# Kernel tuning notes

Hardware: AMD Instinct MI355X
Metric: run time of the kernel (lower is better)

## Reference

```python
import jax, jax.numpy as jnp
import numpy as np

B, D, H, E = 1024, 64, 128, 8192


def setup_inputs() -> dict:
    key = jax.random.key(0)
    ks = jax.random.split(key, 10)
    def w(k, shape, fan_in):
        return jax.random.normal(k, shape, jnp.float32) / np.float32(np.sqrt(fan_in))
    return {
        "mu": jax.random.normal(ks[0], (B, D), jnp.float32),
        "current_edge_index": jax.random.randint(ks[1], (2, E), 0, B),
        "W1": w(ks[2], (D, H), D),   "b1": jnp.zeros((H,), jnp.float32),
        "W2": w(ks[3], (H, H), H),   "b2": jnp.zeros((H,), jnp.float32),
        "Ws1": w(ks[4], (2 * H, H), 2 * H), "bs1": jnp.zeros((H,), jnp.float32),
        "Ws2": w(ks[5], (H, 1), H),  "bs2": jnp.zeros((1,), jnp.float32),
        "Wg1": w(ks[6], (2 * H, H), 2 * H), "bg1": jnp.zeros((H,), jnp.float32),
        "Wg2": w(ks[7], (H, D), H), "bg2": jnp.zeros((D,), jnp.float32),
    }


def _gcn(x, W, b, src, dst, n):
    loop = jnp.arange(n)
    s = jnp.concatenate([src, loop])
    d = jnp.concatenate([dst, loop])
    deg = jax.ops.segment_sum(jnp.ones_like(s, x.dtype), d, num_segments=n)
    dinv = jax.lax.rsqrt(jnp.maximum(deg, 1e-12))
    norm = dinv[s] * dinv[d]                      # [E+n]
    xw = x @ W                                    # [n,H]
    out = jax.ops.segment_sum(xw[s] * norm[:, None], d, num_segments=n)
    return out + b


def _pairwise_scores(h, Ws1, bs1, Ws2, bs2):
    # score_mlp([h_i || h_j]) for all pairs, vectorized: split first-layer weight
    A = h @ Ws1[:H]                               # [B,H] contribution of h_i
    C = h @ Ws1[H:]                               # [B,H] contribution of h_j
    pre = jax.nn.relu(A[:, None, :] + C[None, :, :] + bs1)   # [B,B,H]
    s = (pre @ Ws2)[..., 0] + bs2[0]              # [B,B]
    up = jnp.triu(s, 1)                           # only i<j computed in original
    return up + up.T                              # symmetric, zero diagonal


def _kruskal(scores_np, n):
    iu, ju = np.triu_indices(n, 1)
    w = scores_np[iu, ju]
    order = np.argsort(-w, kind="stable")         # descending, stable like list.sort
    parent = list(range(n))
    rank = [0] * n
    def find(u):
        while parent[u] != u:
            parent[u] = parent[parent[u]]
            u = parent[u]
        return u
    edges = []
    for k in order:
        i, j = int(iu[k]), int(ju[k])
        ri, rj = find(i), find(j)
        if ri == rj:
            continue
        if rank[ri] < rank[rj]:
            parent[ri] = rj
        elif rank[ri] > rank[rj]:
            parent[rj] = ri
        else:
            parent[rj] = ri
            rank[ri] += 1
        edges.append((i, j))
        if len(edges) == n - 1:
            break
    return np.asarray(edges, dtype=np.int64)      # [n-1, 2]


def reference(mu, current_edge_index, W1, b1, W2, b2, Ws1, bs1, Ws2, bs2, Wg1, bg1, Wg2, bg2):
    src, dst = current_edge_index[0], current_edge_index[1]
    h = jax.nn.relu(_gcn(mu, W1, b1, src, dst, B))
    h = jax.nn.relu(_gcn(h, W2, b2, src, dst, B))
    scores = _pairwise_scores(h, Ws1, bs1, Ws2, bs2)          # [B,B]
    mst = _kruskal(np.asarray(scores), B)                     # [B-1,2], i<j
    ei = jnp.asarray(mst[:, 0])
    ej = jnp.asarray(mst[:, 1])
    # bidirectional edge index: src=[i,j,...], dst=[j,i,...]
    new_edge_index = jnp.stack([
        jnp.stack([ei, ej], axis=1).reshape(-1),
        jnp.stack([ej, ei], axis=1).reshape(-1),
    ], axis=0)                                                # [2, 2*(B-1)]
    hp = jnp.concatenate([h[ei], h[ej]], axis=1)              # [B-1, 2H]
    gamma = jnp.tanh(jax.nn.relu(hp @ Wg1 + bg1) @ Wg2 + bg2) # [B-1, D]
    return (new_edge_index, gamma)
```

## Files before the change

### kernel.cpp

```cpp
#include <hip/hip_runtime.h>
#include <hip/hip_bf16.h>
#include <math.h>

#define BN 1024
#define DIN 64
#define HD 128
#define EN 8192
#define SLOTS_STRIDE 64

__global__ void k_init(int* cnt, int* comp, unsigned long long* best, int* mstcnt) {
    int i = blockIdx.x * blockDim.x + threadIdx.x;
    if (i < BN) { cnt[i] = 0; comp[i] = i; best[i] = 0ull; }
    if (i == 0) *mstcnt = 0;
}

__global__ void k_fill(const int* dst, int* cnt, int* slots) {
    int e = blockIdx.x * blockDim.x + threadIdx.x;
    if (e < EN) {
        int d = dst[e];
        int p = atomicAdd(&cnt[d], 1);
        if (p < SLOTS_STRIDE) slots[d * SLOTS_STRIDE + p] = e;
    }
}

__global__ __launch_bounds__(128) void k_finish(int* slots, const int* cnt, float* dinv) {
    __shared__ int buf[128][65];
    int tid = threadIdx.x;
    int t = blockIdx.x * 128 + tid;
    int n = cnt[t];
    if (n > SLOTS_STRIDE) n = SLOTS_STRIDE;
    for (int k = 0; k < n; k++) buf[tid][k] = slots[t * SLOTS_STRIDE + k];
    for (int k = 1; k < n; k++) {
        int v = buf[tid][k];
        int q = k - 1;
        while (q >= 0 && buf[tid][q] > v) { buf[tid][q + 1] = buf[tid][q]; q--; }
        buf[tid][q + 1] = v;
    }
    for (int k = 0; k < n; k++) slots[t * SLOTS_STRIDE + k] = buf[tid][k];
    dinv[t] = 1.0f / sqrtf(fmaxf((float)(n + 1), 1e-12f));
}

__global__ __launch_bounds__(128) void k_mm(const float* x, const float* W, const float* bias,
                                            float* out, int K) {
    __shared__ float xr[HD];
    int row = blockIdx.x, col = threadIdx.x;
    if (col < K) xr[col] = x[row * K + col];
    __syncthreads();
    float acc = bias ? bias[col] : 0.0f;
    for (int k = 0; k < K; k++) acc = fmaf(xr[k], W[k * HD + col], acc);
    out[row * HD + col] = acc;
}

__global__ __launch_bounds__(128) void k_gather(const float* xw, const float* bvec, const int* src,
                                                const int* slots, const int* cnt,
                                                const float* dinv, float* hout) {
    int d = blockIdx.x, t = threadIdx.x;
    float dd = dinv[d];
    float acc = 0.0f;
    int base = d * SLOTS_STRIDE, n = cnt[d];
    if (n > SLOTS_STRIDE) n = SLOTS_STRIDE;
    for (int s = 0; s < n; s++) {
        int e = slots[base + s];
        int sn = src[e];
        acc = fmaf(xw[sn * HD + t], dinv[sn] * dd, acc);
    }
    acc = fmaf(xw[d * HD + t], dd * dd, acc);
    acc += bvec[t];
    hout[d * HD + t] = fmaxf(acc, 0.0f);
}

__global__ __launch_bounds__(256) void k_scores(const float* Aa, const float* Cc,
                                                const float* Ws2, const float* bs2v, float* S) {
    int bi = blockIdx.y, bj = blockIdx.x;
    if (bi > bj) return;
    __shared__ float As[64][68];
    __shared__ float Cs[64][68];
    __shared__ float w2[HD];
    int tid = threadIdx.x;
    int R = bi * 64, Cb = bj * 64;
    if (tid < HD) w2[tid] = Ws2[tid];
    int tx = tid & 15, ty = tid >> 4;
    float acc[4][4] = {};
    for (int half = 0; half < 2; half++) {
        int k0 = half * 64;
        __syncthreads();
        for (int idx = tid; idx < 64 * 64; idx += 256) {
            int row = idx >> 6;
            int kk = idx & 63;
            As[kk][row] = Aa[(R + row) * HD + k0 + kk];
            Cs[kk][row] = Cc[(Cb + row) * HD + k0 + kk];
        }
        __syncthreads();
        for (int kk = 0; kk < 64; kk++) {
            float4 av = *(const float4*)&As[kk][ty * 4];
            float4 cv = *(const float4*)&Cs[kk][tx * 4];
            float wk = w2[k0 + kk];
            float ar[4] = {av.x, av.y, av.z, av.w};
            float cr[4] = {cv.x, cv.y, cv.z, cv.w};
#pragma unroll
            for (int r = 0; r < 4; r++)
#pragma unroll
                for (int q = 0; q < 4; q++) {
                    float tv = fmaxf(ar[r] + cr[q], 0.0f);
                    acc[r][q] = fmaf(tv, wk, acc[r][q]);
                }
        }
    }
    float b2 = bs2v[0];
#pragma unroll
    for (int r = 0; r < 4; r++)
#pragma unroll
        for (int q = 0; q < 4; q++) {
            int gr = R + ty * 4 + r, gc = Cb + tx * 4 + q;
            float v = acc[r][q] + b2;
            if (gr < gc) { S[gr * BN + gc] = v; S[gc * BN + gr] = v; }
            else if (gr == gc) S[gr * BN + gc] = 0.0f;
        }
}

__device__ __forceinline__ unsigned long long edge_key(float w, int i, int j) {
    unsigned u = __float_as_uint(w);
    u = (u & 0x80000000u) ? ~u : (u | 0x80000000u);
    int a = i < j ? i : j, b = i < j ? j : i;
    unsigned packed = (unsigned)(a * BN + b);
    return ((unsigned long long)u << 20) | (unsigned long long)(0xFFFFFu - packed);
}

__global__ __launch_bounds__(256) void k_best(const float* S, const int* comp,
                                              unsigned long long* best) {
    int i = blockIdx.x;
    int ci = comp[i];
    unsigned long long loc = 0ull;
    for (int j = threadIdx.x; j < BN; j += 256) {
        if (comp[j] != ci) {
            unsigned long long key = edge_key(S[i * BN + j], i, j);
            if (key > loc) loc = key;
        }
    }
    __shared__ unsigned long long red[256];
    red[threadIdx.x] = loc;
    __syncthreads();
    for (int s = 128; s > 0; s >>= 1) {
        if (threadIdx.x < s) {
            unsigned long long o = red[threadIdx.x + s];
            if (o > red[threadIdx.x]) red[threadIdx.x] = o;
        }
        __syncthreads();
    }
    if (threadIdx.x == 0 && red[0]) atomicMax(&best[ci], red[0]);
}

__global__ __launch_bounds__(1024) void k_merge(int* comp, unsigned long long* best,
                                                unsigned long long* mst, int* mstcnt) {
    __shared__ int pa[BN], pb[BN];
    int c = threadIdx.x;
    int myComp = comp[c];
    bool root = (myComp == c);
    unsigned long long e = best[c];
    int t = c;
    if (root && e) {
        unsigned packed = 0xFFFFFu - (unsigned)(e & 0xFFFFFu);
        int a = packed >> 10, b = packed & 1023;
        int ca = comp[a], cb = comp[b];
        t = (ca == c) ? cb : ca;
    }
    pa[c] = (root && e) ? t : c;
    __syncthreads();
    bool mutual = root && e && (pa[t] == c);
    int p0 = pa[c];
    if (mutual && c < t) p0 = c;
    __syncthreads();
    pa[c] = p0;
    __syncthreads();
    if (root && e && !(mutual && c > t)) {
        int idx = atomicAdd(mstcnt, 1);
        mst[idx] = e;
    }
    for (int it = 0; it < 10; it++) {
        pb[c] = pa[pa[c]];
        __syncthreads();
        pa[c] = pb[c];
        __syncthreads();
    }
    comp[c] = pa[myComp];
    best[c] = 0ull;
}

__global__ __launch_bounds__(1024) void k_sort(const unsigned long long* mst, float* out, int* pairs) {
    __shared__ unsigned long long s[BN];
    int tid = threadIdx.x;
    s[tid] = (tid < BN - 1) ? mst[tid] : 0ull;
    __syncthreads();
    for (int k = 2; k <= BN; k <<= 1)
        for (int j = k >> 1; j > 0; j >>= 1) {
            int l = tid ^ j;
            if (l > tid) {
                unsigned long long x = s[tid], y = s[l];
                bool up = ((tid & k) == 0);
                if ((x > y) == up) { s[tid] = y; s[l] = x; }
            }
            __syncthreads();
        }
    if (tid < BN - 1) {
        unsigned long long key = s[BN - 1 - tid];
        unsigned packed = 0xFFFFFu - (unsigned)(key & 0xFFFFFu);
        int i = packed >> 10, j2 = packed & 1023;
        out[2 * tid] = (float)i;
        out[2 * tid + 1] = (float)j2;
        out[2046 + 2 * tid] = (float)j2;
        out[2046 + 2 * tid + 1] = (float)i;
        pairs[2 * tid] = i;
        pairs[2 * tid + 1] = j2;
    }
}

__global__ __launch_bounds__(128) void k_gamma(const float* h, const int* pairs,
                                               const float* Wg1, const float* bg1,
                                               const float* Wg2, const float* bg2, float* out) {
    int eidx = blockIdx.x;
    __shared__ float hp[2 * HD];
    __shared__ float z1[HD];
    int t = threadIdx.x;
    int i = pairs[2 * eidx], j = pairs[2 * eidx + 1];
    hp[t] = h[i * HD + t];
    hp[HD + t] = h[j * HD + t];
    __syncthreads();
    float acc = bg1[t];
    for (int k = 0; k < 2 * HD; k++) acc = fmaf(hp[k], Wg1[k * HD + t], acc);
    z1[t] = fmaxf(acc, 0.0f);
    __syncthreads();
    if (t < DIN) {
        float g = bg2[t];
        for (int k = 0; k < HD; k++) g = fmaf(z1[k], Wg2[k * DIN + t], g);
        out[4092 + eidx * DIN + t] = tanhf(g);
    }
}

extern "C" void kernel_launch(void* const* d_in, const int* in_sizes, int n_in,
                              void* d_out, int out_size, void* d_ws, size_t ws_size,
                              hipStream_t stream) {
    const float* mu  = (const float*)d_in[0];
    const int*   ei  = (const int*)d_in[1];
    const float* W1  = (const float*)d_in[2];
    const float* b1  = (const float*)d_in[3];
    const float* W2  = (const float*)d_in[4];
    const float* b2  = (const float*)d_in[5];
    const float* Ws1 = (const float*)d_in[6];
    const float* bs1 = (const float*)d_in[7];
    const float* Ws2 = (const float*)d_in[8];
    const float* bs2 = (const float*)d_in[9];
    const float* Wg1 = (const float*)d_in[10];
    const float* bg1 = (const float*)d_in[11];
    const float* Wg2 = (const float*)d_in[12];
    const float* bg2 = (const float*)d_in[13];
    float* out = (float*)d_out;

    const int* src = ei;
    const int* dst = ei + EN;

    char* ws = (char*)d_ws;
    int*   slots = (int*)(ws);
    int*   cnt   = (int*)(ws + 262144);
    float* dinv  = (float*)(ws + 266240);
    float* S     = (float*)(ws);
    float* xw    = (float*)(ws + 4194304);
    float* h1    = (float*)(ws + 4718592);
    float* h2    = (float*)(ws + 5242880);
    float* Aa    = (float*)(ws + 5767168);
    float* Cc    = (float*)(ws + 6291456);
    int*   comp  = (int*)(ws + 6815744);
    unsigned long long* best = (unsigned long long*)(ws + 6819840);
    unsigned long long* mst  = (unsigned long long*)(ws + 6828032);
    int*   mstcnt = (int*)(ws + 6836224);
    int*   pairs  = (int*)(ws + 6840320);

    k_init<<<4, 256, 0, stream>>>(cnt, comp, best, mstcnt);
    k_fill<<<EN / 256, 256, 0, stream>>>(dst, cnt, slots);
    k_finish<<<BN / 128, 128, 0, stream>>>(slots, cnt, dinv);

    k_mm<<<BN, HD, 0, stream>>>(mu, W1, nullptr, xw, DIN);
    k_gather<<<BN, HD, 0, stream>>>(xw, b1, src, slots, cnt, dinv, h1);
    k_mm<<<BN, HD, 0, stream>>>(h1, W2, nullptr, xw, HD);
    k_gather<<<BN, HD, 0, stream>>>(xw, b2, src, slots, cnt, dinv, h2);

    k_mm<<<BN, HD, 0, stream>>>(h2, Ws1, nullptr, Aa, HD);
    k_mm<<<BN, HD, 0, stream>>>(h2, Ws1 + HD * HD, bs1, Cc, HD);

    k_scores<<<dim3(16, 16), 256, 0, stream>>>(Aa, Cc, Ws2, bs2, S);

    for (int r = 0; r < 10; r++) {
        k_best<<<BN, 256, 0, stream>>>(S, comp, best);
        k_merge<<<1, 1024, 0, stream>>>(comp, best, mst, mstcnt);
    }

    k_sort<<<1, 1024, 0, stream>>>(mst, out, pairs);
    k_gamma<<<BN - 1, HD, 0, stream>>>(h2, pairs, Wg1, bg1, Wg2, bg2, out);
}
```

Before: 179.7 us.

## Fuse entire pipeline into one cooperative persistent kernel with grid syncs

Replaces roughly 30 separate kernel launches with a single cooperative kernel of 256 blocks that separates phases with grid.sync(). It also merges the two Ws1 matmuls, maps only upper-triangle score tiles to blocks, exits the Boruvka rounds early once the MST is complete, and replaces the bitonic sort with a rank-by-counting scatter. The aim is to remove launch overhead and idle blocks between dependent stages. In exchange, each grid-wide barrier has its own cost, the merge step runs on one block of 256 threads instead of 1024, and the slot sort now works in global memory.

```diff
diff --git a/kernel.cpp b/kernel.cpp
--- a/kernel.cpp
+++ b/kernel.cpp
@@ -1,298 +1,345 @@
 #include <hip/hip_runtime.h>
 #include <hip/hip_bf16.h>
+#include <hip/hip_cooperative_groups.h>
 #include <math.h>
+
+namespace cg = cooperative_groups;
 
 #define BN 1024
 #define DIN 64
 #define HD 128
 #define EN 8192
-#define SLOTS_STRIDE 64
-
-__global__ void k_init(int* cnt, int* comp, unsigned long long* best, int* mstcnt) {
-    int i = blockIdx.x * blockDim.x + threadIdx.x;
-    if (i < BN) { cnt[i] = 0; comp[i] = i; best[i] = 0ull; }
-    if (i == 0) *mstcnt = 0;
-}
-
-__global__ void k_fill(const int* dst, int* cnt, int* slots) {
-    int e = blockIdx.x * blockDim.x + threadIdx.x;
-    if (e < EN) {
-        int d = dst[e];
-        int p = atomicAdd(&cnt[d], 1);
-        if (p < SLOTS_STRIDE) slots[d * SLOTS_STRIDE + p] = e;
-    }
-}
-
-__global__ __launch_bounds__(128) void k_finish(int* slots, const int* cnt, float* dinv) {
-    __shared__ int buf[128][65];
-    int tid = threadIdx.x;
-    int t = blockIdx.x * 128 + tid;
-    int n = cnt[t];
-    if (n > SLOTS_STRIDE) n = SLOTS_STRIDE;
-    for (int k = 0; k < n; k++) buf[tid][k] = slots[t * SLOTS_STRIDE + k];
-    for (int k = 1; k < n; k++) {
-        int v = buf[tid][k];
-        int q = k - 1;
-        while (q >= 0 && buf[tid][q] > v) { buf[tid][q + 1] = buf[tid][q]; q--; }
-        buf[tid][q + 1] = v;
-    }
-    for (int k = 0; k < n; k++) slots[t * SLOTS_STRIDE + k] = buf[tid][k];
-    dinv[t] = 1.0f / sqrtf(fmaxf((float)(n + 1), 1e-12f));
-}
-
-__global__ __launch_bounds__(128) void k_mm(const float* x, const float* W, const float* bias,
-                                            float* out, int K) {
-    __shared__ float xr[HD];
-    int row = blockIdx.x, col = threadIdx.x;
-    if (col < K) xr[col] = x[row * K + col];
-    __syncthreads();
-    float acc = bias ? bias[col] : 0.0f;
-    for (int k = 0; k < K; k++) acc = fmaf(xr[k], W[k * HD + col], acc);
-    out[row * HD + col] = acc;
-}
-
-__global__ __launch_bounds__(128) void k_gather(const float* xw, const float* bvec, const int* src,
-                                                const int* slots, const int* cnt,
-                                                const float* dinv, float* hout) {
-    int d = blockIdx.x, t = threadIdx.x;
-    float dd = dinv[d];
-    float acc = 0.0f;
-    int base = d * SLOTS_STRIDE, n = cnt[d];
-    if (n > SLOTS_STRIDE) n = SLOTS_STRIDE;
-    for (int s = 0; s < n; s++) {
-        int e = slots[base + s];
-        int sn = src[e];
-        acc = fmaf(xw[sn * HD + t], dinv[sn] * dd, acc);
-    }
-    acc = fmaf(xw[d * HD + t], dd * dd, acc);
-    acc += bvec[t];
-    hout[d * HD + t] = fmaxf(acc, 0.0f);
-}
-
-__global__ __launch_bounds__(256) void k_scores(const float* Aa, const float* Cc,
-                                                const float* Ws2, const float* bs2v, float* S) {
-    int bi = blockIdx.y, bj = blockIdx.x;
-    if (bi > bj) return;
-    __shared__ float As[64][68];
-    __shared__ float Cs[64][68];
-    __shared__ float w2[HD];
-    int tid = threadIdx.x;
-    int R = bi * 64, Cb = bj * 64;
-    if (tid < HD) w2[tid] = Ws2[tid];
-    int tx = tid & 15, ty = tid >> 4;
-    float acc[4][4] = {};
-    for (int half = 0; half < 2; half++) {
-        int k0 = half * 64;
-        __syncthreads();
-        for (int idx = tid; idx < 64 * 64; idx += 256) {
-            int row = idx >> 6;
-            int kk = idx & 63;
-            As[kk][row] = Aa[(R + row) * HD + k0 + kk];
-            Cs[kk][row] = Cc[(Cb + row) * HD + k0 + kk];
-        }
-        __syncthreads();
-        for (int kk = 0; kk < 64; kk++) {
-            float4 av = *(const float4*)&As[kk][ty * 4];
-            float4 cv = *(const float4*)&Cs[kk][tx * 4];
-            float wk = w2[k0 + kk];
-            float ar[4] = {av.x, av.y, av.z, av.w};
-            float cr[4] = {cv.x, cv.y, cv.z, cv.w};
-#pragma unroll
-            for (int r = 0; r < 4; r++)
-#pragma unroll
-                for (int q = 0; q < 4; q++) {
-                    float tv = fmaxf(ar[r] + cr[q], 0.0f);
-                    acc[r][q] = fmaf(tv, wk, acc[r][q]);
-                }
-        }
-    }
-    float b2 = bs2v[0];
-#pragma unroll
-    for (int r = 0; r < 4; r++)
-#pragma unroll
-        for (int q = 0; q < 4; q++) {
-            int gr = R + ty * 4 + r, gc = Cb + tx * 4 + q;
-            float v = acc[r][q] + b2;
-            if (gr < gc) { S[gr * BN + gc] = v; S[gc * BN + gr] = v; }
-            else if (gr == gc) S[gr * BN + gc] = 0.0f;
-        }
-}
-
-__device__ __forceinline__ unsigned long long edge_key(float w, int i, int j) {
+
+typedef unsigned long long u64;
+
+struct Params {
+    const float* mu; const int* ei;
+    const float* W1; const float* b1; const float* W2; const float* b2;
+    const float* Ws1; const float* bs1; const float* Ws2; const float* bs2;
+    const float* Wg1; const float* bg1; const float* Wg2; const float* bg2;
+    float* out; char* ws;
+};
+
+struct SmemT {
+    union {
+        struct { float As[64][68]; float Cs[64][68]; float w2[HD]; } sc;
+        struct { int pa[BN]; int pb[BN]; } mg;
+        struct { float xr[4][HD]; } mm;
+        struct { float hp[2 * HD]; float z1[HD]; } gm;
+    } u;
+};
+
+__device__ __forceinline__ u64 edge_key(float w, int i, int j) {
     unsigned u = __float_as_uint(w);
     u = (u & 0x80000000u) ? ~u : (u | 0x80000000u);
     int a = i < j ? i : j, b = i < j ? j : i;
     unsigned packed = (unsigned)(a * BN + b);
-    return ((unsigned long long)u << 20) | (unsigned long long)(0xFFFFFu - packed);
-}
-
-__global__ __launch_bounds__(256) void k_best(const float* S, const int* comp,
-                                              unsigned long long* best) {
-    int i = blockIdx.x;
-    int ci = comp[i];
-    unsigned long long loc = 0ull;
-    for (int j = threadIdx.x; j < BN; j += 256) {
-        if (comp[j] != ci) {
-            unsigned long long key = edge_key(S[i * BN + j], i, j);
-            if (key > loc) loc = key;
-        }
-    }
-    __shared__ unsigned long long red[256];
-    red[threadIdx.x] = loc;
+    return ((u64)u << 20) | (u64)(0xFFFFFu - packed);
+}
+
+__device__ void mm_phase(SmemT& sm, int tid, int bid, const float* x, const float* W,
+                         const float* bias, float* out, int K) {
+    int r0 = bid * 4;
+    for (int idx = tid; idx < 4 * K; idx += 256)
+        sm.u.mm.xr[idx / K][idx % K] = x[(r0 + idx / K) * K + idx % K];
     __syncthreads();
-    for (int s = 128; s > 0; s >>= 1) {
-        if (threadIdx.x < s) {
-            unsigned long long o = red[threadIdx.x + s];
-            if (o > red[threadIdx.x]) red[threadIdx.x] = o;
-        }
-        __syncthreads();
-    }
-    if (threadIdx.x == 0 && red[0]) atomicMax(&best[ci], red[0]);
-}
-
-__global__ __launch_bounds__(1024) void k_merge(int* comp, unsigned long long* best,
-                                                unsigned long long* mst, int* mstcnt) {
-    __shared__ int pa[BN], pb[BN];
-    int c = threadIdx.x;
-    int myComp = comp[c];
-    bool root = (myComp == c);
-    unsigned long long e = best[c];
-    int t = c;
-    if (root && e) {
-        unsigned packed = 0xFFFFFu - (unsigned)(e & 0xFFFFFu);
-        int a = packed >> 10, b = packed & 1023;
-        int ca = comp[a], cb = comp[b];
-        t = (ca == c) ? cb : ca;
-    }
-    pa[c] = (root && e) ? t : c;
+    int col = tid & 127;
+    int ra = tid >> 7;
+    float b = bias ? bias[col] : 0.0f;
+    float a0 = b, a1 = b;
+    for (int k = 0; k < K; k++) {
+        float w = W[k * HD + col];
+        a0 = fmaf(sm.u.mm.xr[ra][k], w, a0);
+        a1 = fmaf(sm.u.mm.xr[ra + 2][k], w, a1);
+    }
+    out[(r0 + ra) * HD + col] = a0;
+    out[(r0 + ra + 2) * HD + col] = a1;
+}
+
+__device__ void gather_phase(int tid, int bid, const float* xwv, const float* bvec,
+                             const int* src, const int* slots, const int* cnt,
+                             const float* dinv, float* hout) {
+    int t = tid & 127;
+    for (int p = 0; p < 2; p++) {
+        int d = bid * 4 + (tid >> 7) + p * 2;
+        float dd = dinv[d];
+        float acc = 0.0f;
+        int base = d * 64, n = cnt[d];
+        if (n > 64) n = 64;
+        for (int s = 0; s < n; s++) {
+            int e = slots[base + s];
+            int sn = src[e];
+            acc = fmaf(xwv[sn * HD + t], dinv[sn] * dd, acc);
+        }
+        acc = fmaf(xwv[d * HD + t], dd * dd, acc);
+        acc += bvec[t];
+        hout[d * HD + t] = fmaxf(acc, 0.0f);
+    }
+}
+
+__device__ void merge_block(SmemT& sm, int tid, int* comp, u64* best, u64* mst, int* mstcnt) {
+    int* pa = sm.u.mg.pa;
+    int* pb = sm.u.mg.pb;
+    for (int c = tid; c < BN; c += 256) {
+        int myComp = comp[c];
+        bool root = (myComp == c);
+        u64 e = best[c];
+        int t = c;
+        if (root && e) {
+            unsigned packed = 0xFFFFFu - (unsigned)(e & 0xFFFFFu);
+            int a = packed >> 10, b = packed & 1023;
+            int ca = comp[a], cb = comp[b];
+            t = (ca == c) ? cb : ca;
+        }
+        pa[c] = (root && e) ? t : c;
+    }
     __syncthreads();
-    bool mutual = root && e && (pa[t] == c);
-    int p0 = pa[c];
-    if (mutual && c < t) p0 = c;
+    for (int c = tid; c < BN; c += 256) {
+        int myComp = comp[c];
+        bool root = (myComp == c);
+        u64 e = best[c];
+        int p0 = pa[c];
+        if (root && e) {
+            int t = pa[c];
+            bool mutual = (pa[t] == c);
+            if (mutual && c < t) p0 = c;
+            if (!(mutual && c > t)) {
+                int idx = atomicAdd(mstcnt, 1);
+                mst[idx] = e;
+            }
+        }
+        pb[c] = p0;
+    }
     __syncthreads();
-    pa[c] = p0;
+    for (int c = tid; c < BN; c += 256) pa[c] = pb[c];
     __syncthreads();
-    if (root && e && !(mutual && c > t)) {
-        int idx = atomicAdd(mstcnt, 1);
-        mst[idx] = e;
-    }
     for (int it = 0; it < 10; it++) {
-        pb[c] = pa[pa[c]];
-        __syncthreads();
-        pa[c] = pb[c];
-        __syncthreads();
-    }
-    comp[c] = pa[myComp];
-    best[c] = 0ull;
-}
-
-__global__ __launch_bounds__(1024) void k_sort(const unsigned long long* mst, float* out, int* pairs) {
-    __shared__ unsigned long long s[BN];
-    int tid = threadIdx.x;
-    s[tid] = (tid < BN - 1) ? mst[tid] : 0ull;
-    __syncthreads();
-    for (int k = 2; k <= BN; k <<= 1)
-        for (int j = k >> 1; j > 0; j >>= 1) {
-            int l = tid ^ j;
-            if (l > tid) {
-                unsigned long long x = s[tid], y = s[l];
-                bool up = ((tid & k) == 0);
-                if ((x > y) == up) { s[tid] = y; s[l] = x; }
-            }
-            __syncthreads();
-        }
-    if (tid < BN - 1) {
-        unsigned long long key = s[BN - 1 - tid];
-        unsigned packed = 0xFFFFFu - (unsigned)(key & 0xFFFFFu);
-        int i = packed >> 10, j2 = packed & 1023;
-        out[2 * tid] = (float)i;
-        out[2 * tid + 1] = (float)j2;
-        out[2046 + 2 * tid] = (float)j2;
-        out[2046 + 2 * tid + 1] = (float)i;
-        pairs[2 * tid] = i;
-        pairs[2 * tid + 1] = j2;
-    }
-}
-
-__global__ __launch_bounds__(128) void k_gamma(const float* h, const int* pairs,
-                                               const float* Wg1, const float* bg1,
-                                               const float* Wg2, const float* bg2, float* out) {
-    int eidx = blockIdx.x;
-    __shared__ float hp[2 * HD];
-    __shared__ float z1[HD];
-    int t = threadIdx.x;
-    int i = pairs[2 * eidx], j = pairs[2 * eidx + 1];
-    hp[t] = h[i * HD + t];
-    hp[HD + t] = h[j * HD + t];
-    __syncthreads();
-    float acc = bg1[t];
-    for (int k = 0; k < 2 * HD; k++) acc = fmaf(hp[k], Wg1[k * HD + t], acc);
-    z1[t] = fmaxf(acc, 0.0f);
-    __syncthreads();
-    if (t < DIN) {
-        float g = bg2[t];
-        for (int k = 0; k < HD; k++) g = fmaf(z1[k], Wg2[k * DIN + t], g);
-        out[4092 + eidx * DIN + t] = tanhf(g);
-    }
-}
-
-extern "C" void kernel_launch(void* const* d_in, const int* in_sizes, int n_in,
-                              void* d_out, int out_size, void* d_ws, size_t ws_size,
-                              hipStream_t stream) {
-    const float* mu  = (const float*)d_in[0];
-    const int*   ei  = (const int*)d_in[1];
-    const float* W1  = (const float*)d_in[2];
-    const float* b1  = (const float*)d_in[3];
-    const float* W2  = (const float*)d_in[4];
-    const float* b2  = (const float*)d_in[5];
-    const float* Ws1 = (const float*)d_in[6];
-    const float* bs1 = (const float*)d_in[7];
-    const float* Ws2 = (const float*)d_in[8];
-    const float* bs2 = (const float*)d_in[9];
-    const float* Wg1 = (const float*)d_in[10];
-    const float* bg1 = (const float*)d_in[11];
-    const float* Wg2 = (const float*)d_in[12];
-    const float* bg2 = (const float*)d_in[13];
-    float* out = (float*)d_out;
-
-    const int* src = ei;
-    const int* dst = ei + EN;
-
-    char* ws = (char*)d_ws;
-    int*   slots = (int*)(ws);
+        for (int c = tid; c < BN; c += 256) pb[c] = pa[pa[c]];
+        __syncthreads();
+        for (int c = tid; c < BN; c += 256) pa[c] = pb[c];
+        __syncthreads();
+    }
+    for (int c = tid; c < BN; c += 256) {
+        comp[c] = pa[comp[c]];
+        best[c] = 0ull;
+    }
+}
+
+__global__ __launch_bounds__(256) void k_mega(Params P) {
+    cg::grid_group grid = cg::this_grid();
+    const int tid = threadIdx.x;
+    const int bid = blockIdx.x;
+    const int gid = bid * 256 + tid;
+    __shared__ SmemT sm;
+
+    char* ws = P.ws;
+    int*   slots = (int*)ws;
     int*   cnt   = (int*)(ws + 262144);
     float* dinv  = (float*)(ws + 266240);
-    float* S     = (float*)(ws);
+    float* S     = (float*)ws;
     float* xw    = (float*)(ws + 4194304);
     float* h1    = (float*)(ws + 4718592);
     float* h2    = (float*)(ws + 5242880);
     float* Aa    = (float*)(ws + 5767168);
     float* Cc    = (float*)(ws + 6291456);
     int*   comp  = (int*)(ws + 6815744);
-    unsigned long long* best = (unsigned long long*)(ws + 6819840);
-    unsigned long long* mst  = (unsigned long long*)(ws + 6828032);
+    u64*   best  = (u64*)(ws + 6819840);
+    u64*   mst   = (u64*)(ws + 6828032);
     int*   mstcnt = (int*)(ws + 6836224);
     int*   pairs  = (int*)(ws + 6840320);
 
-    k_init<<<4, 256, 0, stream>>>(cnt, comp, best, mstcnt);
-    k_fill<<<EN / 256, 256, 0, stream>>>(dst, cnt, slots);
-    k_finish<<<BN / 128, 128, 0, stream>>>(slots, cnt, dinv);
-
-    k_mm<<<BN, HD, 0, stream>>>(mu, W1, nullptr, xw, DIN);
-    k_gather<<<BN, HD, 0, stream>>>(xw, b1, src, slots, cnt, dinv, h1);
-    k_mm<<<BN, HD, 0, stream>>>(h1, W2, nullptr, xw, HD);
-    k_gather<<<BN, HD, 0, stream>>>(xw, b2, src, slots, cnt, dinv, h2);
-
-    k_mm<<<BN, HD, 0, stream>>>(h2, Ws1, nullptr, Aa, HD);
-    k_mm<<<BN, HD, 0, stream>>>(h2, Ws1 + HD * HD, bs1, Cc, HD);
-
-    k_scores<<<dim3(16, 16), 256, 0, stream>>>(Aa, Cc, Ws2, bs2, S);
+    const int* src = P.ei;
+    const int* dst = P.ei + EN;
+
+    if (gid < BN) { cnt[gid] = 0; comp[gid] = gid; best[gid] = 0ull; }
+    if (gid == 0) *mstcnt = 0;
+    grid.sync();
+
+    if (gid < EN) {
+        int d = dst[gid];
+        int p = atomicAdd(&cnt[d], 1);
+        if (p < 64) slots[d * 64 + p] = gid;
+    }
+    grid.sync();
+
+    if (gid < BN) {
+        int n = cnt[gid];
+        if (n > 64) n = 64;
+        int b = gid * 64;
+        for (int k = 1; k < n; k++) {
+            int v = slots[b + k];
+            int q = k - 1;
+            while (q >= 0 && slots[b + q] > v) { slots[b + q + 1] = slots[b + q]; q--; }
+            slots[b + q + 1] = v;
+        }
+        dinv[gid] = 1.0f / sqrtf(fmaxf((float)(n + 1), 1e-12f));
+    }
+    grid.sync();
+
+    mm_phase(sm, tid, bid, P.mu, P.W1, nullptr, xw, DIN);
+    grid.sync();
+    gather_phase(tid, bid, xw, P.b1, src, slots, cnt, dinv, h1);
+    grid.sync();
+    mm_phase(sm, tid, bid, h1, P.W2, nullptr, xw, HD);
+    grid.sync();
+    gather_phase(tid, bid, xw, P.b2, src, slots, cnt, dinv, h2);
+    grid.sync();
+
+    {
+        int r0 = bid * 4;
+        for (int idx = tid; idx < 4 * HD; idx += 256)
+            sm.u.mm.xr[idx / HD][idx % HD] = h2[(r0 + idx / HD) * HD + idx % HD];
+        __syncthreads();
+        int col = tid & 127;
+        int ra = tid >> 7;
+        float bc = P.bs1[col];
+        float aA0 = 0.0f, aA1 = 0.0f, aC0 = bc, aC1 = bc;
+        for (int k = 0; k < HD; k++) {
+            float wa = P.Ws1[k * HD + col];
+            float wc = P.Ws1[(HD + k) * HD + col];
+            aA0 = fmaf(sm.u.mm.xr[ra][k], wa, aA0);
+            aA1 = fmaf(sm.u.mm.xr[ra + 2][k], wa, aA1);
+            aC0 = fmaf(sm.u.mm.xr[ra][k], wc, aC0);
+            aC1 = fmaf(sm.u.mm.xr[ra + 2][k], wc, aC1);
+        }
+        Aa[(r0 + ra) * HD + col] = aA0;
+        Aa[(r0 + ra + 2) * HD + col] = aA1;
+        Cc[(r0 + ra) * HD + col] = aC0;
+        Cc[(r0 + ra + 2) * HD + col] = aC1;
+    }
+    grid.sync();
+
+    if (bid < 136) {
+        int bi = 0, rem = bid;
+        while (rem >= 16 - bi) { rem -= 16 - bi; bi++; }
+        int bj = bi + rem;
+        int R = bi * 64, Cb = bj * 64;
+        if (tid < HD) sm.u.sc.w2[tid] = P.Ws2[tid];
+        int tx = tid & 15, ty = tid >> 4;
+        float acc[4][4] = {};
+        for (int half = 0; half < 2; half++) {
+            int k0 = half * 64;
+            __syncthreads();
+            for (int idx = tid; idx < 64 * 64; idx += 256) {
+                int row = idx >> 6;
+                int kk = idx & 63;
+                sm.u.sc.As[kk][row] = Aa[(R + row) * HD + k0 + kk];
+                sm.u.sc.Cs[kk][row] = Cc[(Cb + row) * HD + k0 + kk];
+            }
+            __syncthreads();
+            for (int kk = 0; kk < 64; kk++) {
+                float4 av = *(const float4*)&sm.u.sc.As[kk][ty * 4];
+                float4 cv = *(const float4*)&sm.u.sc.Cs[kk][tx * 4];
+                float wk = sm.u.sc.w2[k0 + kk];
+                float ar[4] = {av.x, av.y, av.z, av.w};
+                float cr[4] = {cv.x, cv.y, cv.z, cv.w};
+#pragma unroll
+                for (int r = 0; r < 4; r++)
+#pragma unroll
+                    for (int q = 0; q < 4; q++) {
+                        float tv = fmaxf(ar[r] + cr[q], 0.0f);
+                        acc[r][q] = fmaf(tv, wk, acc[r][q]);
+                    }
+            }
+        }
+        float b2 = P.bs2[0];
+#pragma unroll
+        for (int r = 0; r < 4; r++)
+#pragma unroll
+            for (int q = 0; q < 4; q++) {
+                int gr = R + ty * 4 + r, gc = Cb + tx * 4 + q;
+                float v = acc[r][q] + b2;
+                if (gr < gc) { S[gr * BN + gc] = v; S[gc * BN + gr] = v; }
+                else if (gr == gc) S[gr * BN + gc] = 0.0f;
+            }
+    }
+    grid.sync();
 
     for (int r = 0; r < 10; r++) {
-        k_best<<<BN, 256, 0, stream>>>(S, comp, best);
-        k_merge<<<1, 1024, 0, stream>>>(comp, best, mst, mstcnt);
-    }
-
-    k_sort<<<1, 1024, 0, stream>>>(mst, out, pairs);
-    k_gamma<<<BN - 1, HD, 0, stream>>>(h2, pairs, Wg1, bg1, Wg2, bg2, out);
-}
+        if (*(volatile int*)mstcnt >= BN - 1) break;
+        {
+            int i = gid >> 6, lane = gid & 63;
+            int ci = comp[i];
+            u64 loc = 0ull;
+            const float* Srow = S + i * BN;
+            for (int j = lane; j < BN; j += 64)
+                if (comp[j] != ci) {
+                    u64 key = edge_key(Srow[j], i, j);
+                    if (key > loc) loc = key;
+                }
+            for (int off = 32; off > 0; off >>= 1) {
+                u64 o = __shfl_xor(loc, off);
+                if (o > loc) loc = o;
+            }
+            if (lane == 0 && loc) atomicMax(&best[ci], loc);
+        }
+        grid.sync();
+        if (bid == 0) merge_block(sm, tid, comp, best, mst, mstcnt);
+        grid.sync();
+    }
+
+    {
+        int e = gid >> 6, lane = gid & 63;
+        if (e < BN - 1) {
+            u64 mykey = mst[e];
+            int cg_ = 0;
+            for (int f = lane; f < BN - 1; f += 64) cg_ += (mst[f] > mykey) ? 1 : 0;
+            for (int off = 32; off > 0; off >>= 1) cg_ += __shfl_xor(cg_, off);
+            if (lane == 0) {
+                int rk = cg_;
+                unsigned packed = 0xFFFFFu - (unsigned)(mykey & 0xFFFFFu);
+                int i = packed >> 10, j2 = packed & 1023;
+                P.out[2 * rk] = (float)i;
+                P.out[2 * rk + 1] = (float)j2;
+                P.out[2046 + 2 * rk] = (float)j2;
+                P.out[2046 + 2 * rk + 1] = (float)i;
+                pairs[2 * rk] = i;
+                pairs[2 * rk + 1] = j2;
+            }
+        }
+    }
+    grid.sync();
+
+    for (int e = bid; e < BN - 1; e += 256) {
+        int i = pairs[2 * e], j = pairs[2 * e + 1];
+        sm.u.gm.hp[tid] = (tid < HD) ? h2[i * HD + tid] : h2[j * HD + (tid - HD)];
+        __syncthreads();
+        if (tid < HD) {
+            float acc = P.bg1[tid];
+            for (int k = 0; k < 2 * HD; k++) acc = fmaf(sm.u.gm.hp[k], P.Wg1[k * HD + tid], acc);
+            sm.u.gm.z1[tid] = fmaxf(acc, 0.0f);
+        }
+        __syncthreads();
+        if (tid < DIN) {
+            float g = P.bg2[tid];
+            for (int k = 0; k < HD; k++) g = fmaf(sm.u.gm.z1[k], P.Wg2[k * DIN + tid], g);
+            P.out[4092 + e * DIN + tid] = tanhf(g);
+        }
+        __syncthreads();
+    }
+}
+
+extern "C" void kernel_launch(void* const* d_in, const int* in_sizes, int n_in,
+                              void* d_out, int out_size, void* d_ws, size_t ws_size,
+                              hipStream_t stream) {
+    Params P;
+    P.mu  = (const float*)d_in[0];
+    P.ei  = (const int*)d_in[1];
+    P.W1  = (const float*)d_in[2];
+    P.b1  = (const float*)d_in[3];
+    P.W2  = (const float*)d_in[4];
+    P.b2  = (const float*)d_in[5];
+    P.Ws1 = (const float*)d_in[6];
+    P.bs1 = (const float*)d_in[7];
+    P.Ws2 = (const float*)d_in[8];
+    P.bs2 = (const float*)d_in[9];
+    P.Wg1 = (const float*)d_in[10];
+    P.bg1 = (const float*)d_in[11];
+    P.Wg2 = (const float*)d_in[12];
+    P.bg2 = (const float*)d_in[13];
+    P.out = (float*)d_out;
+    P.ws  = (char*)d_ws;
+
+    void* args[] = { &P };
+    hipLaunchCooperativeKernel((const void*)k_mega, dim3(256), dim3(256), args, 0, stream);
+}
```

Result: slower. 512.6 us (+185.2%).
